# Kernel optimization log

Hardware: AMD Instinct MI355X
Metric: run time of the kernel (lower is better)

Reference implementation:

```python
import jax, jax.numpy as jnp
import numpy as np

B, L, F = 8, 2048, 4
DM, DI, N, DCONV, DTRANK = 320, 1280, 16, 8, 20  # d_model, d_inner, d_state, d_conv, dt_rank
NBLK = 4


def setup_inputs() -> dict:
    key = jax.random.key(0)
    ks = jax.random.split(key, 24)
    s = 0.05
    inp = {
        "x": jax.random.uniform(ks[0], (B, L, F), jnp.float32),
        "fc_w": jax.random.normal(ks[1], (320, 4), jnp.float32) * s,
        "fc_b": jnp.zeros((320,), jnp.float32),
        "blk_lin_w": jax.random.normal(ks[2], (NBLK, 320, 320), jnp.float32) * s,
        "blk_lin_b": jnp.zeros((NBLK, 320), jnp.float32),
        "blk_inproj_w": jax.random.normal(ks[3], (NBLK, 2 * DI, DM), jnp.float32) * s,
        "blk_conv_w": jax.random.normal(ks[4], (NBLK, DI, DCONV), jnp.float32) * s,
        "blk_conv_b": jnp.zeros((NBLK, DI), jnp.float32),
        "blk_xproj_w": jax.random.normal(ks[5], (NBLK, DTRANK + 2 * N, DI), jnp.float32) * s,
        "blk_dtproj_w": jax.random.normal(ks[6], (NBLK, DI, DTRANK), jnp.float32) * s,
        "blk_dtproj_b": jnp.full((NBLK, DI), -4.0, jnp.float32),  # softplus(-4) ~ 0.018, stable dt
        "blk_A_log": jnp.tile(jnp.log(jnp.arange(1, N + 1, dtype=jnp.float32)), (NBLK, DI, 1)),
        "blk_D": jnp.ones((NBLK, DI), jnp.float32),
        "blk_outproj_w": jax.random.normal(ks[7], (NBLK, DM, DI), jnp.float32) * s,
        "s1_w1": jax.random.normal(ks[8], (512, 320), jnp.float32) * s,
        "s1_b1": jnp.zeros((512,), jnp.float32),
        "s1_w2": jax.random.normal(ks[9], (512, 512), jnp.float32) * s,
        "s1_b2": jnp.zeros((512,), jnp.float32),
        "s1_w3": jax.random.normal(ks[10], (1, 512), jnp.float32) * s,
        "s1_b3": jnp.zeros((1,), jnp.float32),
    }
    return inp


def _mamba(u, inproj_w, conv_w, conv_b, xproj_w, dtproj_w, dtproj_b, A_log, D):
    # u: (B, L, DM)
    xz = u @ inproj_w.T                       # (B, L, 2*DI)
    x, z = jnp.split(xz, 2, axis=-1)
    # causal depthwise conv1d over time
    xc = jnp.transpose(x, (0, 2, 1))          # (B, DI, L)
    xc = jax.lax.conv_general_dilated(
        xc, conv_w[:, None, :], (1,), [(DCONV - 1, 0)],
        feature_group_count=DI, dimension_numbers=("NCH", "OIH", "NCH"))
    xc = xc + conv_b[None, :, None]
    x = jax.nn.silu(jnp.transpose(xc, (0, 2, 1)))  # (B, L, DI)
    dbc = x @ xproj_w.T                        # (B, L, DTRANK + 2N)
    dt, Bm, Cm = jnp.split(dbc, [DTRANK, DTRANK + N], axis=-1)
    delta = jax.nn.softplus(dt @ dtproj_w.T + dtproj_b)  # (B, L, DI)
    A = -jnp.exp(A_log)                        # (DI, N)

    def step(h, inp):
        xt, dt_t, Bt, Ct = inp                 # (B,DI),(B,DI),(B,N),(B,N)
        dA = jnp.exp(dt_t[..., None] * A)      # (B, DI, N)
        h = dA * h + (dt_t * xt)[..., None] * Bt[:, None, :]
        y = jnp.einsum("bdn,bn->bd", h, Ct)
        return h, y

    h0 = jnp.zeros((u.shape[0], DI, N), x.dtype)
    xs = (jnp.swapaxes(x, 0, 1), jnp.swapaxes(delta, 0, 1),
          jnp.swapaxes(Bm, 0, 1), jnp.swapaxes(Cm, 0, 1))
    _, ys = jax.lax.scan(step, h0, xs)         # ys: (L, B, DI)
    y = jnp.swapaxes(ys, 0, 1) + x * D         # (B, L, DI)
    y = y * jax.nn.silu(z)
    return y


def reference(x, fc_w, fc_b, blk_lin_w, blk_lin_b, blk_inproj_w, blk_conv_w,
              blk_conv_b, blk_xproj_w, blk_dtproj_w, blk_dtproj_b, blk_A_log,
              blk_D, blk_outproj_w, s1_w1, s1_b1, s1_w2, s1_b2, s1_w3, s1_b3):
    seq_len = x.shape[1]
    start_max = jnp.max(x[:, :, 2])
    xn = jnp.stack([x[:, :, 0] / 255.0,
                    x[:, :, 1] / 255.0,
                    x[:, :, 2] / start_max,
                    x[:, :, 3]], axis=-1)
    out = xn @ fc_w.T + fc_b                   # (B, L, 320)
    for i in range(NBLK):
        out = jnp.tanh(out @ blk_lin_w[i].T + blk_lin_b[i])
        out = _mamba(out, blk_inproj_w[i], blk_conv_w[i], blk_conv_b[i],
                     blk_xproj_w[i], blk_dtproj_w[i], blk_dtproj_b[i],
                     blk_A_log[i], blk_D[i]) @ blk_outproj_w[i].T
        out = jax.nn.elu(out)                  # dropout p=1e-6 -> identity (eval)
    h = out[:, -1, :]                          # (B, 320)
    h = jax.nn.relu(h @ s1_w1.T + s1_b1)
    h = jax.nn.relu(h @ s1_w2.T + s1_b2)
    h = h @ s1_w3.T + s1_b3                    # (B, 1)
    scale = start_max / (1.0 + np.log(seq_len))
    h = h.at[:, 0].multiply(scale)
    return jax.nn.relu(h)
```

## Files before the change

### kernel.cpp

```cpp
#include <hip/hip_runtime.h>
#include <math.h>

#define BSZ 8
#define LSZ 2048
#define DMV 320
#define DIV 1280
#define NST 16
#define DCV 8
#define DTR 20
#define NBLKV 4
#define MTOT (BSZ*LSZ)
#define NCHUNK 64
#define CLEN 32
#define DBLD 56

typedef __attribute__((ext_vector_type(8))) short short8;
typedef __attribute__((ext_vector_type(8))) unsigned short ushort8;
typedef __attribute__((ext_vector_type(4))) float floatx4;

__device__ inline unsigned short f2bf(float f) {
    union { float f; unsigned u; } v; v.f = f;
    unsigned r = v.u + 0x7FFFu + ((v.u >> 16) & 1u);
    return (unsigned short)(r >> 16);
}
__device__ inline float bf2f(unsigned short b) {
    union { unsigned u; float f; } v; v.u = ((unsigned)b) << 16;
    return v.f;
}

__device__ __forceinline__ void gload_lds16(unsigned short* l, const unsigned short* g) {
    __builtin_amdgcn_global_load_lds(
        (const __attribute__((address_space(1))) unsigned int*)g,
        (__attribute__((address_space(3))) unsigned int*)l, 16, 0, 0);
}

__global__ __launch_bounds__(256) void convert_kernel(
    const float* __restrict__ src, unsigned short* __restrict__ dst, long n4) {
    long i = (long)blockIdx.x * 256 + threadIdx.x;
    if (i >= n4) return;
    float4 v = *(const float4*)(src + i * 4);
    unsigned short o[4] = {f2bf(v.x), f2bf(v.y), f2bf(v.z), f2bf(v.w)};
    *(unsigned long long*)(dst + i * 4) = *(unsigned long long*)o;
}

__global__ __launch_bounds__(256) void convert_dtw_kernel(
    const float* __restrict__ src, unsigned short* __restrict__ dst) {
    int i = blockIdx.x * 256 + threadIdx.x;
    if (i >= NBLKV * DIV * 32) return;
    int l = i / (DIV * 32), rem = i % (DIV * 32);
    int d = rem >> 5, j = rem & 31;
    dst[i] = (j < DTR) ? f2bf(src[((long)l * DIV + d) * DTR + j]) : (unsigned short)0;
}

__global__ __launch_bounds__(256) void convert_xp_kernel(
    const float* __restrict__ src, unsigned short* __restrict__ dst) {
    int i = blockIdx.x * 256 + threadIdx.x;
    if (i >= NBLKV * 64 * DIV) return;
    int l = i / (64 * DIV), rem = i % (64 * DIV);
    int n = rem / DIV, k = rem % DIV;
    dst[i] = (n < DTR + 2 * NST) ? f2bf(src[((long)l * (DTR + 2 * NST) + n) * DIV + k])
                                 : (unsigned short)0;
}

__global__ __launch_bounds__(256) void convert_t2_kernel(
    const float* __restrict__ src, unsigned short* __restrict__ dst, int N, int K) {
    int i = blockIdx.x * 256 + threadIdx.x;
    if (i >= N * K) return;
    int n = i / K, k = i % K;
    dst[((k >> 1) * N + n) * 2 + (k & 1)] = f2bf(src[i]);
}

__global__ void init_sm_kernel(float* sm) {
    if (threadIdx.x == 0) ((int*)sm)[0] = 0;
}

__global__ void reduce_max_kernel(const float* __restrict__ x, float* sm) {
    int idx = blockIdx.x * blockDim.x + threadIdx.x;
    float v = 0.f;
    for (int i = idx; i < MTOT; i += gridDim.x * blockDim.x)
        v = fmaxf(v, x[i * 4 + 2]);
    #pragma unroll
    for (int off = 32; off > 0; off >>= 1)
        v = fmaxf(v, __shfl_xor(v, off, 64));
    if ((threadIdx.x & 63) == 0)
        atomicMax((int*)sm, __float_as_int(v));
}

__global__ __launch_bounds__(256) void fc_kernel(
    const float* __restrict__ x, const float* __restrict__ fw,
    const float* __restrict__ fb, const float* __restrict__ sm,
    unsigned short* __restrict__ u) {
    int o = blockIdx.x * 64 + (threadIdx.x & 63);
    long m = (long)blockIdx.y * 4 + (threadIdx.x >> 6);
    float inv_sm = 1.0f / sm[0];
    float x0 = x[m * 4 + 0] * (1.0f / 255.0f);
    float x1 = x[m * 4 + 1] * (1.0f / 255.0f);
    float x2 = x[m * 4 + 2] * inv_sm;
    float x3 = x[m * 4 + 3];
    float acc = fb[o];
    acc = fmaf(x0, fw[o * 4 + 0], acc);
    acc = fmaf(x1, fw[o * 4 + 1], acc);
    acc = fmaf(x2, fw[o * 4 + 2], acc);
    acc = fmaf(x3, fw[o * 4 + 3], acc);
    u[m * DMV + o] = f2bf(acc);
}

template<int ACT, int BM, int BN, int KB, typename TOUT>
__global__ __launch_bounds__(256) void gemm_mfma_kernel(
    const unsigned short* __restrict__ X, const unsigned short* __restrict__ W,
    const float* __restrict__ bias, TOUT* __restrict__ Y,
    int N, int K, long ldx, long ldy)
{
    constexpr int WMT = (BM == 128 && BN == 128) ? 4 : 2;
    constexpr int WNT = (BM == 64 && BN == 64) ? 2 : 4;
    constexpr int CPR = KB / 8;
    constexpr int CMSK = CPR - 1;
    constexpr int NCX = BM * CPR / 256;
    constexpr int NCW = BN * CPR / 256;
    __shared__ unsigned short Xs[BM * KB];
    __shared__ unsigned short Ws[BN * KB];

    int tid = threadIdx.x;
    int wave = tid >> 6, lane = tid & 63;
    int quad = lane >> 4, l15 = lane & 15;
    int wmbase, wnbase;
    if (BM == 128 && BN == 128)      { wmbase = (wave & 1) * 64; wnbase = (wave >> 1) * 64; }
    else if (BM == 128 && BN == 64)  { wmbase = wave * 32;       wnbase = 0; }
    else                             { wmbase = (wave & 1) * 32; wnbase = (wave >> 1) * 32; }

    int nbx = gridDim.x;
    long by; int bx;
    if ((gridDim.y & 7) == 0) {
        long lin = (long)blockIdx.y * nbx + blockIdx.x;
        int xcd = (int)(lin & 7);
        long j = lin >> 3;
        bx = (int)(j % nbx);
        by = (j / nbx) * 8 + xcd;
    } else {
        bx = blockIdx.x;
        by = blockIdx.y;
    }
    long m0 = by * BM;
    int n0 = bx * BN;

    floatx4 acc[WMT][WNT];
    #pragma unroll
    for (int i = 0; i < WMT; i++)
        #pragma unroll
        for (int j = 0; j < WNT; j++)
            acc[i][j] = (floatx4){0.f, 0.f, 0.f, 0.f};

    const unsigned short* Xb = X + m0 * ldx;
    const unsigned short* Wb = W + (long)n0 * K;

    for (int k0 = 0; k0 < K; k0 += KB) {
        #pragma unroll
        for (int j = 0; j < NCX; j++) {
            int s = (wave * NCX + j) * 64 + lane;
            int r = s / CPR, c = s % CPR;
            int cg = c ^ (r & CMSK);
            gload_lds16(&Xs[(wave * NCX + j) * 512],
                        Xb + (long)r * ldx + k0 + cg * 8);
        }
        #pragma unroll
        for (int j = 0; j < NCW; j++) {
            int s = (wave * NCW + j) * 64 + lane;
            int r = s / CPR, c = s % CPR;
            int cg = c ^ (r & CMSK);
            gload_lds16(&Ws[(wave * NCW + j) * 512],
                        Wb + (long)r * K + k0 + cg * 8);
        }
        __syncthreads();
        #pragma unroll
        for (int kk = 0; kk < KB; kk += 32) {
            short8 af[WMT], bfr[WNT];
            #pragma unroll
            for (int i = 0; i < WMT; i++) {
                int R = wmbase + i * 16 + l15;
                int cp = (kk / 8 + quad) ^ (R & CMSK);
                af[i] = *(short8*)&Xs[R * KB + cp * 8];
            }
            #pragma unroll
            for (int j = 0; j < WNT; j++) {
                int R = wnbase + j * 16 + l15;
                int cp = (kk / 8 + quad) ^ (R & CMSK);
                bfr[j] = *(short8*)&Ws[R * KB + cp * 8];
            }
            #pragma unroll
            for (int i = 0; i < WMT; i++)
                #pragma unroll
                for (int j = 0; j < WNT; j++)
                    acc[i][j] = __builtin_amdgcn_mfma_f32_16x16x32_bf16(
                        af[i], bfr[j], acc[i][j], 0, 0, 0);
        }
        __syncthreads();
    }

    #pragma unroll
    for (int i = 0; i < WMT; i++) {
        long mb = m0 + wmbase + i * 16 + quad * 4;
        #pragma unroll
        for (int j = 0; j < WNT; j++) {
            int n = n0 + wnbase + j * 16 + l15;
            if (n >= N) continue;
            float bv = bias ? bias[n] : 0.f;
            #pragma unroll
            for (int r = 0; r < 4; r++) {
                float v = acc[i][j][r] + bv;
                if (ACT == 1) v = tanhf(v);
                else if (ACT == 3) v = (v > 0.f) ? v : expm1f(v);
                else if (ACT == 4) v = (v > 20.f) ? v : __logf(1.0f + __expf(v));
                if constexpr (sizeof(TOUT) == 2)
                    Y[(mb + r) * ldy + n] = f2bf(v);
                else
                    Y[(mb + r) * ldy + n] = v;
            }
        }
    }
}

__global__ __launch_bounds__(512) void head_kernel(
    const unsigned short* __restrict__ u,
    const unsigned short* __restrict__ w1t, const float* __restrict__ b1,
    const unsigned short* __restrict__ w2t, const float* __restrict__ b2,
    const float* __restrict__ w3, const float* __restrict__ b3,
    const float* __restrict__ sm, float* __restrict__ out)
{
    __shared__ float xs[DMV];
    __shared__ float h1s[512];
    __shared__ float red[8];
    int b = blockIdx.x;
    int tid = threadIdx.x;
    const unsigned short* xr = u + ((long)b * LSZ + (LSZ - 1)) * DMV;
    if (tid < DMV) xs[tid] = bf2f(xr[tid]);
    __syncthreads();

    float acc = 0.f;
    #pragma unroll 8
    for (int kk = 0; kk < DMV / 2; kk++) {
        unsigned wv = *(const unsigned*)&w1t[((long)kk * 512 + tid) * 2];
        acc = fmaf(xs[2 * kk],     bf2f((unsigned short)(wv & 0xffffu)), acc);
        acc = fmaf(xs[2 * kk + 1], bf2f((unsigned short)(wv >> 16)), acc);
    }
    h1s[tid] = fmaxf(acc + b1[tid], 0.f);
    __syncthreads();

    acc = 0.f;
    #pragma unroll 8
    for (int kk = 0; kk < 256; kk++) {
        unsigned wv = *(const unsigned*)&w2t[((long)kk * 512 + tid) * 2];
        acc = fmaf(h1s[2 * kk],     bf2f((unsigned short)(wv & 0xffffu)), acc);
        acc = fmaf(h1s[2 * kk + 1], bf2f((unsigned short)(wv >> 16)), acc);
    }
    float h2 = fmaxf(acc + b2[tid], 0.f);

    float part = h2 * w3[tid];
    #pragma unroll
    for (int off = 32; off > 0; off >>= 1) part += __shfl_xor(part, off, 64);
    if ((tid & 63) == 0) red[tid >> 6] = part;
    __syncthreads();
    if (tid == 0) {
        float s = b3[0];
        #pragma unroll
        for (int w = 0; w < 8; w++) s += red[w];
        float scale = sm[0] / 8.624618986159398f;
        out[b] = fmaxf(s * scale, 0.f);
    }
}

#define TCONV 32
__global__ __launch_bounds__(256) void conv_kernel(
    const unsigned short* __restrict__ xz, const float* __restrict__ cw,
    const float* __restrict__ cb, unsigned short* __restrict__ xc)
{
    int d = blockIdx.x * 256 + threadIdx.x;
    int lb = blockIdx.z;
    int l0 = blockIdx.y * TCONV;
    long base = (long)lb * LSZ + l0;

    float w[8];
    #pragma unroll
    for (int k = 0; k < 8; k++) w[k] = cw[d * 8 + k];
    float bc = cb[d];

    float win[8];
    #pragma unroll
    for (int i = 0; i < 7; i++) {
        int l = l0 - 7 + i;
        win[i] = (l >= 0) ? bf2f(xz[(base - 7 + i) * 2560 + d]) : 0.f;
    }
    #pragma unroll
    for (int s = 0; s < TCONV; s++) {
        win[7] = bf2f(xz[(base + s) * 2560 + d]);
        float acc = bc;
        #pragma unroll
        for (int k = 0; k < 8; k++) acc = fmaf(win[k], w[k], acc);
        float sv = acc / (1.0f + __expf(-acc));
        xc[(base + s) * DIV + d] = f2bf(sv);
        #pragma unroll
        for (int k = 0; k < 7; k++) win[k] = win[k + 1];
    }
}

__device__ inline void pow_ladder(float p, float* pw) {
    pw[0] = p;
    pw[1] = pw[0] * pw[0];
    pw[2] = pw[1] * pw[0];
    pw[3] = pw[1] * pw[1];
    pw[4] = pw[3] * pw[0];
    pw[5] = pw[3] * pw[1];
    pw[6] = pw[3] * pw[2];
    pw[7] = pw[3] * pw[3];
    #pragma unroll
    for (int k = 8; k < 16; k++) pw[k] = pw[7] * pw[k - 8];
}

__global__ __launch_bounds__(256) void scan_local_kernel(
    const unsigned short* __restrict__ xc, unsigned short* xz,
    const unsigned short* __restrict__ dbc, const unsigned short* __restrict__ delta,
    const float* __restrict__ A_log, const float* __restrict__ Dp,
    unsigned short* __restrict__ hfin, float* __restrict__ sumd)
{
    __shared__ float S[CLEN * 32];
    int lb = blockIdx.z;
    int ch = blockIdx.y;
    int d = blockIdx.x * 256 + threadIdx.x;
    int tid = threadIdx.x;

    float a[NST], h[NST];
    #pragma unroll
    for (int n = 0; n < NST; n++) {
        a[n] = -__expf(A_log[d * NST + n]);
        h[n] = 0.f;
    }
    float a0 = a[0];
    bool geo = true;
    #pragma unroll
    for (int n = 1; n < NST; n++)
        geo = geo && (fabsf(a[n] - (float)(n + 1) * a0) <= 1e-4f * (float)(n + 1));
    float Dd = Dp[d];

    long tok0 = (long)lb * LSZ + ch * CLEN;
    for (int i = tid; i < CLEN * 32; i += 256) {
        int r = i >> 5, c = i & 31;
        S[i] = bf2f(dbc[(tok0 + r) * DBLD + 20 + c]);
    }
    __syncthreads();

    float sd = 0.f;
    if (__all(geo)) {
        for (int l = 0; l < CLEN; l++) {
            long m = tok0 + l;
            const float* row = &S[l * 32];
            float dl = bf2f(delta[m * DIV + d]);
            sd += dl;
            float xv = bf2f(xc[m * DIV + d]);
            float db = dl * xv;
            float pw[NST];
            pow_ladder(__expf(dl * a0), pw);
            float y = 0.f;
            #pragma unroll
            for (int n = 0; n < NST; n++) {
                h[n] = fmaf(pw[n], h[n], db * row[n]);
                y = fmaf(h[n], row[16 + n], y);
            }
            y = fmaf(xv, Dd, y);
            xz[m * 2560 + d] = f2bf(y);
        }
    } else {
        for (int l = 0; l < CLEN; l++) {
            long m = tok0 + l;
            const float* row = &S[l * 32];
            float dl = bf2f(delta[m * DIV + d]);
            sd += dl;
            float xv = bf2f(xc[m * DIV + d]);
            float db = dl * xv;
            float y = 0.f;
            #pragma unroll
            for (int n = 0; n < NST; n++) {
                float dA = __expf(dl * a[n]);
                h[n] = fmaf(dA, h[n], db * row[n]);
                y = fmaf(h[n], row[16 + n], y);
            }
            y = fmaf(xv, Dd, y);
            xz[m * 2560 + d] = f2bf(y);
        }
    }

    long cidx = ((long)lb * NCHUNK + ch) * DIV + d;
    #pragma unroll
    for (int n = 0; n < NST; n++) hfin[cidx * NST + n] = f2bf(h[n]);
    sumd[cidx] = sd;
}

__global__ __launch_bounds__(256) void scan_prefix_kernel(
    unsigned short* __restrict__ hfin, const float* __restrict__ sumd,
    const float* __restrict__ A_log, int Bc)
{
    long g = (long)blockIdx.x * 256 + threadIdx.x;
    int n = (int)(g & (NST - 1));
    long t = g >> 4;
    int d = (int)(t % DIV);
    int lb = (int)(t / DIV);
    if (lb >= Bc) return;

    float a = -__expf(A_log[d * NST + n]);
    float s = 0.f;
    for (int c = 0; c < NCHUNK; c++) {
        long cidx = ((long)lb * NCHUNK + c) * DIV + d;
        float hl = bf2f(hfin[cidx * NST + n]);
        float P = __expf(a * sumd[cidx]);
        hfin[cidx * NST + n] = f2bf(s);
        s = fmaf(P, s, hl);
    }
}

__global__ __launch_bounds__(256) void scan_fix_kernel(
    unsigned short* xz, const unsigned short* __restrict__ dbc,
    const unsigned short* __restrict__ delta,
    const float* __restrict__ A_log, const unsigned short* __restrict__ hfin)
{
    __shared__ float S[CLEN * 16];
    int lb = blockIdx.z;
    int ch = blockIdx.y;
    int d = blockIdx.x * 256 + threadIdx.x;
    int tid = threadIdx.x;

    float a[NST], hin[NST];
    #pragma unroll
    for (int n = 0; n < NST; n++) a[n] = -__expf(A_log[d * NST + n]);
    float a0 = a[0];
    bool geo = true;
    #pragma unroll
    for (int n = 1; n < NST; n++)
        geo = geo && (fabsf(a[n] - (float)(n + 1) * a0) <= 1e-4f * (float)(n + 1));

    long cidx = ((long)lb * NCHUNK + ch) * DIV + d;
    #pragma unroll
    for (int n = 0; n < NST; n++) hin[n] = bf2f(hfin[cidx * NST + n]);

    long tok0 = (long)lb * LSZ + ch * CLEN;
    for (int i = tid; i < CLEN * 16; i += 256) {
        int r = i >> 4, c = i & 15;
        S[i] = bf2f(dbc[(tok0 + r) * DBLD + 36 + c]);
    }
    __syncthreads();

    float cum = 0.f;
    if (__all(geo)) {
        for (int l = 0; l < CLEN; l++) {
            long m = tok0 + l;
            const float* row = &S[l * 16];
            cum += bf2f(delta[m * DIV + d]);
            float pw[NST];
            pow_ladder(__expf(cum * a0), pw);
            float fix = 0.f;
            #pragma unroll
            for (int n = 0; n < NST; n++)
                fix = fmaf(hin[n] * pw[n], row[n], fix);
            float y = bf2f(xz[m * 2560 + d]) + fix;
            float zv = bf2f(xz[m * 2560 + 1280 + d]);
            float sz = zv / (1.0f + __expf(-zv));
            xz[m * 2560 + d] = f2bf(y * sz);
        }
    } else {
        for (int l = 0; l < CLEN; l++) {
            long m = tok0 + l;
            const float* row = &S[l * 16];
            cum += bf2f(delta[m * DIV + d]);
            float fix = 0.f;
            #pragma unroll
            for (int n = 0; n < NST; n++)
                fix = fmaf(hin[n] * __expf(cum * a[n]), row[n], fix);
            float y = bf2f(xz[m * 2560 + d]) + fix;
            float zv = bf2f(xz[m * 2560 + 1280 + d]);
            float sz = zv / (1.0f + __expf(-zv));
            xz[m * 2560 + d] = f2bf(y * sz);
        }
    }
}

extern "C" void kernel_launch(void* const* d_in, const int* in_sizes, int n_in,
                              void* d_out, int out_size, void* d_ws, size_t ws_size,
                              hipStream_t stream) {
    const float* x        = (const float*)d_in[0];
    const float* fc_w     = (const float*)d_in[1];
    const float* fc_b     = (const float*)d_in[2];
    const float* lin_w    = (const float*)d_in[3];
    const float* lin_b    = (const float*)d_in[4];
    const float* inproj_w = (const float*)d_in[5];
    const float* conv_w   = (const float*)d_in[6];
    const float* conv_b   = (const float*)d_in[7];
    const float* xproj_w  = (const float*)d_in[8];
    const float* dtproj_w = (const float*)d_in[9];
    const float* dtproj_b = (const float*)d_in[10];
    const float* A_log    = (const float*)d_in[11];
    const float* Dp       = (const float*)d_in[12];
    const float* outproj_w= (const float*)d_in[13];
    const float* s1_w1    = (const float*)d_in[14];
    const float* s1_b1    = (const float*)d_in[15];
    const float* s1_w2    = (const float*)d_in[16];
    const float* s1_b2    = (const float*)d_in[17];
    const float* s1_w3    = (const float*)d_in[18];
    const float* s1_b3    = (const float*)d_in[19];

    const long NLIN = (long)NBLKV * DMV * DMV;
    const long NINP = (long)NBLKV * 2 * DIV * DMV;
    const long NXPP = (long)NBLKV * 64 * DIV;
    const long NOUT = (long)NBLKV * DMV * DIV;
    const long NDTW = (long)NBLKV * DIV * 32;
    const long NHW1 = (long)512 * DMV;
    const long NHW2 = (long)512 * 512;

    const long FIXED = 256 +
                       (NLIN + NINP + NXPP + NOUT + NDTW + NHW1 + NHW2) * 2 + 256;
    const long PER_BATCH = (long)LSZ * (DMV + DMV + 2 * DIV + DIV) * 2
                         + (long)LSZ * DBLD * 2
                         + (long)LSZ * DIV * 2
                         + (long)NCHUNK * DIV * NST * 2
                         + (long)NCHUNK * DIV * 4;
    int Bc = 8;
    while (Bc > 1 && (size_t)(FIXED + (long)Bc * PER_BATCH) > ws_size)
        Bc >>= 1;
    int nchunk_b = BSZ / Bc;
    long Mc = (long)Bc * LSZ;

    char* p = (char*)d_ws;
    float* sm = (float*)p;           p += 256;
    unsigned short* wlin = (unsigned short*)p; p += NLIN * 2;
    unsigned short* winp = (unsigned short*)p; p += NINP * 2;
    unsigned short* wxp  = (unsigned short*)p; p += NXPP * 2;
    unsigned short* wout = (unsigned short*)p; p += NOUT * 2;
    unsigned short* wdt  = (unsigned short*)p; p += NDTW * 2;
    unsigned short* w1t  = (unsigned short*)p; p += NHW1 * 2;
    unsigned short* w2t  = (unsigned short*)p; p += NHW2 * 2;
    unsigned short* u  = (unsigned short*)p;   p += Mc * DMV * 2;
    unsigned short* t  = (unsigned short*)p;   p += Mc * DMV * 2;
    unsigned short* xz = (unsigned short*)p;   p += Mc * 2560 * 2;
    unsigned short* xc = (unsigned short*)p;   p += Mc * DIV * 2;
    unsigned short* dbc = (unsigned short*)p;  p += Mc * DBLD * 2;
    unsigned short* delta = (unsigned short*)p; p += Mc * DIV * 2;
    unsigned short* hfin = (unsigned short*)p; p += (long)Bc * NCHUNK * DIV * NST * 2;
    float* sumd = (float*)p;

    convert_kernel<<<(unsigned)((NLIN / 4 + 255) / 256), 256, 0, stream>>>(lin_w, wlin, NLIN / 4);
    convert_kernel<<<(unsigned)((NINP / 4 + 255) / 256), 256, 0, stream>>>(inproj_w, winp, NINP / 4);
    convert_kernel<<<(unsigned)((NOUT / 4 + 255) / 256), 256, 0, stream>>>(outproj_w, wout, NOUT / 4);
    convert_xp_kernel<<<(unsigned)((NXPP + 255) / 256), 256, 0, stream>>>(xproj_w, wxp);
    convert_dtw_kernel<<<(unsigned)((NDTW + 255) / 256), 256, 0, stream>>>(dtproj_w, wdt);
    convert_t2_kernel<<<(unsigned)((NHW1 + 255) / 256), 256, 0, stream>>>(s1_w1, w1t, 512, DMV);
    convert_t2_kernel<<<(unsigned)((NHW2 + 255) / 256), 256, 0, stream>>>(s1_w2, w2t, 512, 512);

    init_sm_kernel<<<1, 64, 0, stream>>>(sm);
    reduce_max_kernel<<<32, 256, 0, stream>>>(x, sm);

    for (int c = 0; c < nchunk_b; c++) {
        int b0 = c * Bc;
        fc_kernel<<<dim3(5, (unsigned)(Mc / 4)), 256, 0, stream>>>(
            x + (long)b0 * LSZ * 4, fc_w, fc_b, sm, u);

        for (int i = 0; i < NBLKV; i++) {
            const float* lb  = lin_b    + (long)i * DMV;
            const float* cw  = conv_w   + (long)i * DIV * DCV;
            const float* cb  = conv_b   + (long)i * DIV;
            const float* dpb = dtproj_b + (long)i * DIV;
            const float* al  = A_log    + (long)i * DIV * NST;
            const float* dd  = Dp       + (long)i * DIV;

            gemm_mfma_kernel<1, 128, 64, 64, unsigned short>
                <<<dim3(5, (unsigned)(Mc / 128)), 256, 0, stream>>>(
                u, wlin + (long)i * DMV * DMV, lb, t, DMV, DMV, DMV, DMV);
            gemm_mfma_kernel<0, 128, 128, 64, unsigned short>
                <<<dim3(20, (unsigned)(Mc / 128)), 256, 0, stream>>>(
                t, winp + (long)i * 2 * DIV * DMV, nullptr, xz, 2 * DIV, DMV, DMV, 2 * DIV);
            conv_kernel<<<dim3(5, LSZ / TCONV, Bc), 256, 0, stream>>>(xz, cw, cb, xc);
            gemm_mfma_kernel<0, 64, 64, 64, unsigned short>
                <<<dim3(1, (unsigned)(Mc / 64)), 256, 0, stream>>>(
                xc, wxp + (long)i * 64 * DIV, nullptr, dbc,
                DTR + 2 * NST, DIV, DIV, DBLD);
            gemm_mfma_kernel<4, 128, 128, 32, unsigned short>
                <<<dim3(10, (unsigned)(Mc / 128)), 256, 0, stream>>>(
                dbc, wdt + (long)i * DIV * 32, dpb, delta, DIV, 32, DBLD, DIV);
            scan_local_kernel<<<dim3(5, NCHUNK, Bc), 256, 0, stream>>>(
                xc, xz, dbc, delta, al, dd, hfin, sumd);
            scan_prefix_kernel<<<dim3(Bc * 80), 256, 0, stream>>>(hfin, sumd, al, Bc);
            scan_fix_kernel<<<dim3(5, NCHUNK, Bc), 256, 0, stream>>>(
                xz, dbc, delta, al, hfin);
            gemm_mfma_kernel<3, 128, 64, 64, unsigned short>
                <<<dim3(5, (unsigned)(Mc / 128)), 256, 0, stream>>>(
                xz, wout + (long)i * DMV * DIV, nullptr, u, DMV, DIV, 2 * DIV, DMV);
        }

        head_kernel<<<Bc, 512, 0, stream>>>(u, w1t, s1_b1, w2t, s1_b2,
                                            s1_w3, s1_b3, sm, (float*)d_out + b0);
    }
}
```

Measured before the change: 1.174 ms.

## Retile in_proj and x_proj GEMMs and pack two channels per conv thread

The GEMM template gains a thread-count parameter and new wave layouts. The in_proj GEMM moves to 256x128 tiles with 512 threads, and the x_proj GEMM moves to 32x64 tiles so more blocks are launched. The depthwise conv kernel now has each of 128 threads handle two adjacent channels, using 32-bit packed bf16 loads and stores. The aim is more reuse per block on the large GEMM, better occupancy on the skinny GEMM, and fewer memory transactions in the conv, at the cost of higher register and LDS pressure for the 512-thread tile.

```diff
diff --git a/kernel.cpp b/kernel.cpp
--- a/kernel.cpp
+++ b/kernel.cpp
@@ -105,18 +105,24 @@
     u[m * DMV + o] = f2bf(acc);
 }
 
-template<int ACT, int BM, int BN, int KB, typename TOUT>
-__global__ __launch_bounds__(256) void gemm_mfma_kernel(
+template<int ACT, int BM, int BN, int KB, int T, typename TOUT>
+__global__ __launch_bounds__(T) void gemm_mfma_kernel(
     const unsigned short* __restrict__ X, const unsigned short* __restrict__ W,
     const float* __restrict__ bias, TOUT* __restrict__ Y,
     int N, int K, long ldx, long ldy)
 {
-    constexpr int WMT = (BM == 128 && BN == 128) ? 4 : 2;
-    constexpr int WNT = (BM == 64 && BN == 64) ? 2 : 4;
+    constexpr int WMT = (BM == 256) ? 4
+                      : (BM == 128 && BN == 128) ? 4
+                      : (BM == 128 && BN == 64) ? 2
+                      : (BM == 64) ? 2 : 1;
+    constexpr int WNT = (BM == 256) ? 4
+                      : (BM == 128 && BN == 128) ? 4
+                      : (BM == 128 && BN == 64) ? 4
+                      : (BM == 64) ? 2 : 2;
     constexpr int CPR = KB / 8;
     constexpr int CMSK = CPR - 1;
-    constexpr int NCX = BM * CPR / 256;
-    constexpr int NCW = BN * CPR / 256;
+    constexpr int NCX = BM * CPR / T;
+    constexpr int NCW = BN * CPR / T;
     __shared__ unsigned short Xs[BM * KB];
     __shared__ unsigned short Ws[BN * KB];
 
@@ -124,9 +130,11 @@
     int wave = tid >> 6, lane = tid & 63;
     int quad = lane >> 4, l15 = lane & 15;
     int wmbase, wnbase;
-    if (BM == 128 && BN == 128)      { wmbase = (wave & 1) * 64; wnbase = (wave >> 1) * 64; }
-    else if (BM == 128 && BN == 64)  { wmbase = wave * 32;       wnbase = 0; }
-    else                             { wmbase = (wave & 1) * 32; wnbase = (wave >> 1) * 32; }
+    if (BM == 256)                        { wmbase = (wave & 3) * 64; wnbase = (wave >> 2) * 64; }
+    else if (BM == 128 && BN == 128)      { wmbase = (wave & 1) * 64; wnbase = (wave >> 1) * 64; }
+    else if (BM == 128 && BN == 64)       { wmbase = wave * 32;       wnbase = 0; }
+    else if (BM == 64)                    { wmbase = (wave & 1) * 32; wnbase = (wave >> 1) * 32; }
+    else                                  { wmbase = (wave & 1) * 16; wnbase = (wave >> 1) * 32; }
 
     int nbx = gridDim.x;
     long by; int bx;
@@ -269,36 +277,44 @@
 }
 
 #define TCONV 32
-__global__ __launch_bounds__(256) void conv_kernel(
+__global__ __launch_bounds__(128) void conv_kernel(
     const unsigned short* __restrict__ xz, const float* __restrict__ cw,
     const float* __restrict__ cb, unsigned short* __restrict__ xc)
 {
-    int d = blockIdx.x * 256 + threadIdx.x;
+    int d0 = blockIdx.x * 256 + threadIdx.x * 2;
     int lb = blockIdx.z;
     int l0 = blockIdx.y * TCONV;
     long base = (long)lb * LSZ + l0;
 
-    float w[8];
-    #pragma unroll
-    for (int k = 0; k < 8; k++) w[k] = cw[d * 8 + k];
-    float bc = cb[d];
-
-    float win[8];
+    float w0[8], w1[8];
+    #pragma unroll
+    for (int k = 0; k < 8; k++) { w0[k] = cw[d0 * 8 + k]; w1[k] = cw[(d0 + 1) * 8 + k]; }
+    float bc0 = cb[d0], bc1 = cb[d0 + 1];
+
+    float a0[8], a1[8];
     #pragma unroll
     for (int i = 0; i < 7; i++) {
         int l = l0 - 7 + i;
-        win[i] = (l >= 0) ? bf2f(xz[(base - 7 + i) * 2560 + d]) : 0.f;
+        if (l >= 0) {
+            unsigned v = *(const unsigned*)&xz[(base - 7 + i) * 2560 + d0];
+            a0[i] = bf2f((unsigned short)(v & 0xffffu));
+            a1[i] = bf2f((unsigned short)(v >> 16));
+        } else { a0[i] = 0.f; a1[i] = 0.f; }
     }
     #pragma unroll
     for (int s = 0; s < TCONV; s++) {
-        win[7] = bf2f(xz[(base + s) * 2560 + d]);
-        float acc = bc;
-        #pragma unroll
-        for (int k = 0; k < 8; k++) acc = fmaf(win[k], w[k], acc);
-        float sv = acc / (1.0f + __expf(-acc));
-        xc[(base + s) * DIV + d] = f2bf(sv);
-        #pragma unroll
-        for (int k = 0; k < 7; k++) win[k] = win[k + 1];
+        unsigned v = *(const unsigned*)&xz[(base + s) * 2560 + d0];
+        a0[7] = bf2f((unsigned short)(v & 0xffffu));
+        a1[7] = bf2f((unsigned short)(v >> 16));
+        float c0 = bc0, c1 = bc1;
+        #pragma unroll
+        for (int k = 0; k < 8; k++) { c0 = fmaf(a0[k], w0[k], c0); c1 = fmaf(a1[k], w1[k], c1); }
+        float s0 = c0 / (1.0f + __expf(-c0));
+        float s1 = c1 / (1.0f + __expf(-c1));
+        unsigned o = (unsigned)f2bf(s0) | ((unsigned)f2bf(s1) << 16);
+        *(unsigned*)&xc[(base + s) * DIV + d0] = o;
+        #pragma unroll
+        for (int k = 0; k < 7; k++) { a0[k] = a0[k + 1]; a1[k] = a1[k + 1]; }
     }
 }
 
@@ -567,18 +583,18 @@
             const float* al  = A_log    + (long)i * DIV * NST;
             const float* dd  = Dp       + (long)i * DIV;
 
-            gemm_mfma_kernel<1, 128, 64, 64, unsigned short>
+            gemm_mfma_kernel<1, 128, 64, 64, 256, unsigned short>
                 <<<dim3(5, (unsigned)(Mc / 128)), 256, 0, stream>>>(
                 u, wlin + (long)i * DMV * DMV, lb, t, DMV, DMV, DMV, DMV);
-            gemm_mfma_kernel<0, 128, 128, 64, unsigned short>
-                <<<dim3(20, (unsigned)(Mc / 128)), 256, 0, stream>>>(
+            gemm_mfma_kernel<0, 256, 128, 64, 512, unsigned short>
+                <<<dim3(20, (unsigned)(Mc / 256)), 512, 0, stream>>>(
                 t, winp + (long)i * 2 * DIV * DMV, nullptr, xz, 2 * DIV, DMV, DMV, 2 * DIV);
-            conv_kernel<<<dim3(5, LSZ / TCONV, Bc), 256, 0, stream>>>(xz, cw, cb, xc);
-            gemm_mfma_kernel<0, 64, 64, 64, unsigned short>
-                <<<dim3(1, (unsigned)(Mc / 64)), 256, 0, stream>>>(
+            conv_kernel<<<dim3(5, LSZ / TCONV, Bc), 128, 0, stream>>>(xz, cw, cb, xc);
+            gemm_mfma_kernel<0, 32, 64, 64, 256, unsigned short>
+                <<<dim3(1, (unsigned)(Mc / 32)), 256, 0, stream>>>(
                 xc, wxp + (long)i * 64 * DIV, nullptr, dbc,
                 DTR + 2 * NST, DIV, DIV, DBLD);
-            gemm_mfma_kernel<4, 128, 128, 32, unsigned short>
+            gemm_mfma_kernel<4, 128, 128, 32, 256, unsigned short>
                 <<<dim3(10, (unsigned)(Mc / 128)), 256, 0, stream>>>(
                 dbc, wdt + (long)i * DIV * 32, dpb, delta, DIV, 32, DBLD, DIV);
             scan_local_kernel<<<dim3(5, NCHUNK, Bc), 256, 0, stream>>>(
@@ -586,7 +602,7 @@
             scan_prefix_kernel<<<dim3(Bc * 80), 256, 0, stream>>>(hfin, sumd, al, Bc);
             scan_fix_kernel<<<dim3(5, NCHUNK, Bc), 256, 0, stream>>>(
                 xz, dbc, delta, al, hfin);
-            gemm_mfma_kernel<3, 128, 64, 64, unsigned short>
+            gemm_mfma_kernel<3, 128, 64, 64, 256, unsigned short>
                 <<<dim3(5, (unsigned)(Mc / 128)), 256, 0, stream>>>(
                 xz, wout + (long)i * DMV * DIV, nullptr, u, DMV, DIV, 2 * DIV, DMV);
         }
```

Measured after the change: 1.119 ms, median of 2. 4.7% less time.
